# Performance work log

Measured on AMD Instinct MI355X. Metric: run time of the kernel, lower is better.

The kernel has to match this reference:

```python
import jax, jax.numpy as jnp
import numpy as np

B, C, H, W = 4, 64, 128, 128
O, K = 64, 3
STRIDE, PAD = 1, 1
K2 = K * K


def conv2d(x, w, b):
    out = jax.lax.conv_general_dilated(
        x, w, (STRIDE, STRIDE), [(PAD, PAD), (PAD, PAD)],
        dimension_numbers=('NCHW', 'OIHW', 'NCHW'))
    return out + b[None, :, None, None]


def setup_inputs() -> dict:
    key = jax.random.key(0)
    ks = jax.random.split(key, 6)
    return {
        'x': jax.random.normal(ks[0], (B, C, H, W), jnp.float32),
        'offset_w': jax.random.normal(ks[1], (2 * K2, C, K, K), jnp.float32) * 0.01,
        'offset_b': jax.random.normal(ks[2], (2 * K2,), jnp.float32) * 0.01,
        'mask_w': jax.random.normal(ks[3], (K2, C, K, K), jnp.float32) * 0.01,
        'mask_b': jnp.zeros((K2,), jnp.float32),
        'deform_w': jax.random.normal(ks[4], (O, C, K, K), jnp.float32) * (1.0 / np.sqrt(C * K2)),
        'deform_b': jax.random.normal(ks[5], (O,), jnp.float32) * 0.01,
    }


def _deform_conv(x, offset, mask, w, b):
    Bn, Cn, Hin, Win = x.shape
    Ho, Wo = offset.shape[2], offset.shape[3]
    off = offset.reshape(Bn, K2, 2, Ho, Wo)
    ky = jnp.repeat(jnp.arange(K), K)   # kernel row offset per location k
    kx = jnp.tile(jnp.arange(K), K)     # kernel col offset per location k
    yo = jnp.arange(Ho) * STRIDE - PAD
    xo = jnp.arange(Wo) * STRIDE - PAD
    # sampling positions [B,K2,Ho,Wo]
    py = off[:, :, 0] + ky[None, :, None, None] + yo[None, None, :, None]
    px = off[:, :, 1] + kx[None, :, None, None] + xo[None, None, None, :]
    y0 = jnp.floor(py)
    x0 = jnp.floor(px)
    wy1 = py - y0  # fractional weights
    wx1 = px - x0
    y0i = y0.astype(jnp.int32)
    x0i = x0.astype(jnp.int32)
    x_flat = x.reshape(Bn, Cn, Hin * Win)

    def corner(yi, xi, wgt):
        valid = (yi >= 0) & (yi < Hin) & (xi >= 0) & (xi < Win)
        yc = jnp.clip(yi, 0, Hin - 1)
        xc = jnp.clip(xi, 0, Win - 1)
        idx = (yc * Win + xc).reshape(Bn, -1)
        g = jnp.take_along_axis(x_flat, idx[:, None, :], axis=2)
        g = g.reshape(Bn, Cn, K2, Ho, Wo)
        return g * (wgt * valid)[:, None]

    val = (corner(y0i, x0i, (1 - wy1) * (1 - wx1))
           + corner(y0i, x0i + 1, (1 - wy1) * wx1)
           + corner(y0i + 1, x0i, wy1 * (1 - wx1))
           + corner(y0i + 1, x0i + 1, wy1 * wx1))
    val = val * mask[:, None]  # modulate, broadcast over channels
    out = jnp.einsum('bckhw,ock->bohw', val, w.reshape(w.shape[0], Cn, K2))
    return out + b[None, :, None, None]


def reference(x, offset_w, offset_b, mask_w, mask_b, deform_w, deform_b):
    offset = conv2d(x, offset_w, offset_b)
    mask = jax.nn.sigmoid(conv2d(x, mask_w, mask_b))
    return _deform_conv(x, offset, mask, deform_w, deform_b)
```

## Files before the change

kernel.cpp:

```cpp
#include <hip/hip_runtime.h>
#include <hip/hip_bf16.h>
#include <math.h>

#define BB 4
#define CC 64
#define HH 128
#define WW 128
#define HW 16384
#define CHW (CC*HW)

typedef __bf16 bf16;
typedef __attribute__((ext_vector_type(8))) __bf16 bf16x8;
typedef __attribute__((ext_vector_type(4))) __bf16 bf16x4;
typedef __attribute__((ext_vector_type(4))) float f32x4;
typedef __attribute__((ext_vector_type(4))) unsigned short u16x4;

#define MFMA(a, b, c) __builtin_amdgcn_mfma_f32_16x16x32_bf16((a), (b), (c), 0, 0, 0)

__global__ __launch_bounds__(256) void k_pre(const float* __restrict__ x,
        bf16* __restrict__ xt,
        const float* __restrict__ dw, const float* __restrict__ ow,
        const float* __restrict__ mw,
        bf16* __restrict__ wfd_hi, bf16* __restrict__ wfd_lo,
        bf16* __restrict__ wfo_hi, bf16* __restrict__ wfo_lo) {
    __shared__ float tile[64][65];
    if (blockIdx.x < 1024) {
        int b    = blockIdx.x >> 8;
        int s0   = (blockIdx.x & 255) * 64;
        int lane = threadIdx.x & 63;
        int w    = threadIdx.x >> 6;
        const float* xb = x + (size_t)b * CHW;
        #pragma unroll
        for (int r = 0; r < 16; ++r) {
            int c = w * 16 + r;
            tile[c][lane] = xb[(size_t)c * HW + s0 + lane];
        }
        __syncthreads();
        bf16* xtb = xt + (size_t)b * CHW;
        #pragma unroll
        for (int r = 0; r < 16; ++r) {
            int si = w * 16 + r;
            xtb[(size_t)(s0 + si) * 64 + lane] = (bf16)tile[lane][si];
        }
    } else {
        int idx = (blockIdx.x - 1024) * 256 + threadIdx.x;
        if (idx < 36864) {
            int j    = idx & 7;
            int lane = (idx >> 3) & 63;
            int ks   = (idx >> 9) % 18;
            int nt   = idx / (512 * 18);
            int n    = nt * 16 + (lane & 15);
            int kglob = ks * 32 + (lane >> 4) * 8 + j;
            int kk = kglob >> 6, c = kglob & 63;
            float w = dw[(n * 64 + c) * 9 + kk];
            bf16 h = (bf16)w;
            wfd_hi[idx] = h;
            wfd_lo[idx] = (bf16)(w - (float)h);
        } else {
            int idx2 = idx - 36864;
            int j    = idx2 & 7;
            int lane = (idx2 >> 3) & 63;
            int ks   = (idx2 >> 9) % 18;
            int nt   = idx2 / (512 * 18);
            int ch   = nt * 16 + (lane & 15);
            int kglob = ks * 32 + (lane >> 4) * 8 + j;
            int kk = kglob >> 6, c = kglob & 63;
            float w = 0.0f;
            if (ch < 18)      w = ow[(ch * 64 + c) * 9 + kk];
            else if (ch < 27) w = mw[((ch - 18) * 64 + c) * 9 + kk];
            bf16 h = (bf16)w;
            wfo_hi[idx2] = h;
            wfo_lo[idx2] = (bf16)(w - (float)h);
        }
    }
}

__global__ __launch_bounds__(256) void k_fused(const bf16* __restrict__ xt,
        const bf16* __restrict__ wfo_hi, const bf16* __restrict__ wfo_lo,
        const bf16* __restrict__ wfd_hi,
        const float* __restrict__ ob, const float* __restrict__ mb,
        const float* __restrict__ db, float* __restrict__ out) {
    __shared__ __align__(16) bf16 a_s[18 * 64 * 8];
    __shared__ float om_s[27 * 64];
    __shared__ __align__(8) bf16 sampw[576 * 4];
    __shared__ __align__(8) unsigned short sampo[576 * 4];

    int pos0 = blockIdx.x * 64;
    int wo0 = pos0 & 127;
    int ho  = (pos0 >> 7) & 127;
    int b   = pos0 >> 14;
    int t = threadIdx.x, wave = t >> 6, lane = t & 63;
    int m = lane & 15, g = lane >> 4;
    const bf16* xtb = xt + (size_t)b * CHW;

    {
        int st = wave;
        f32x4 acc0 = {0.f, 0.f, 0.f, 0.f};
        f32x4 acc1 = {0.f, 0.f, 0.f, 0.f};
        const bf16x8* bh0 = (const bf16x8*)wfo_hi + lane;
        const bf16x8* bl0 = (const bf16x8*)wfo_lo + lane;
        const bf16x8* bh1 = (const bf16x8*)wfo_hi + 18 * 64 + lane;
        const bf16x8* bl1 = (const bf16x8*)wfo_lo + 18 * 64 + lane;
        #pragma unroll
        for (int kk = 0; kk < 9; ++kk) {
            int y  = ho + kk / 3 - 1;
            int xx = wo0 + st * 16 + m + (kk % 3) - 1;
            bf16x8 ae = {};
            bf16x8 ao = {};
            if ((unsigned)y < 128u && (unsigned)xx < 128u) {
                const bf16* bp = xtb + ((size_t)(y * 128 + xx) << 6);
                ae = *(const bf16x8*)(bp + g * 8);
                ao = *(const bf16x8*)(bp + 32 + g * 8);
            }
            int ks0 = 2 * kk, ks1 = 2 * kk + 1;
            acc0 = MFMA(ae, bh0[ks0 * 64], acc0);
            acc0 = MFMA(ae, bl0[ks0 * 64], acc0);
            acc0 = MFMA(ao, bh0[ks1 * 64], acc0);
            acc0 = MFMA(ao, bl0[ks1 * 64], acc0);
            acc1 = MFMA(ae, bh1[ks0 * 64], acc1);
            acc1 = MFMA(ae, bl1[ks0 * 64], acc1);
            acc1 = MFMA(ao, bh1[ks1 * 64], acc1);
            acc1 = MFMA(ao, bl1[ks1 * 64], acc1);
        }
        int p64 = st * 16 + g * 4;
        float bias0 = ob[m];
        #pragma unroll
        for (int r = 0; r < 4; ++r)
            om_s[m * 64 + p64 + r] = acc0[r] + bias0;
        int ch1 = 16 + m;
        if (ch1 < 27) {
            float bias1 = (ch1 < 18) ? ob[ch1] : mb[ch1 - 18];
            #pragma unroll
            for (int r = 0; r < 4; ++r) {
                float v = acc1[r] + bias1;
                if (ch1 >= 18) v = 1.0f / (1.0f + __expf(-v));
                om_s[ch1 * 64 + p64 + r] = v;
            }
        }
    }
    __syncthreads();

    for (int task = t; task < 576; task += 256) {
        int p64 = task / 9, k = task - p64 * 9;
        float dy = om_s[(2 * k) * 64 + p64];
        float dx = om_s[(2 * k + 1) * 64 + p64];
        float mk = om_s[(18 + k) * 64 + p64];
        float py = (float)(ho - 1 + k / 3) + dy;
        float px = (float)(wo0 + p64 - 1 + (k % 3)) + dx;
        float y0f = floorf(py), x0f = floorf(px);
        float fy = py - y0f, fx = px - x0f;
        int y0 = (int)y0f, x0 = (int)x0f;
        int y1 = y0 + 1,  x1 = x0 + 1;
        bool vy0 = (unsigned)y0 < 128u, vy1 = (unsigned)y1 < 128u;
        bool vx0 = (unsigned)x0 < 128u, vx1 = (unsigned)x1 < 128u;
        int y0c = min(max(y0, 0), 127), y1c = min(max(y1, 0), 127);
        int x0c = min(max(x0, 0), 127), x1c = min(max(x1, 0), 127);
        bf16x4 wv;
        wv.x = (bf16)((vy0 && vx0) ? mk * (1.f - fy) * (1.f - fx) : 0.f);
        wv.y = (bf16)((vy0 && vx1) ? mk * (1.f - fy) * fx         : 0.f);
        wv.z = (bf16)((vy1 && vx0) ? mk * fy * (1.f - fx)         : 0.f);
        wv.w = (bf16)((vy1 && vx1) ? mk * fy * fx                 : 0.f);
        u16x4 ov;
        ov.x = (unsigned short)(y0c * 128 + x0c);
        ov.y = (unsigned short)(y0c * 128 + x1c);
        ov.z = (unsigned short)(y1c * 128 + x0c);
        ov.w = (unsigned short)(y1c * 128 + x1c);
        *(bf16x4*)&sampw[task * 4] = wv;
        *(u16x4*)&sampo[task * 4] = ov;
    }
    __syncthreads();

    const bf16x8* bhd = (const bf16x8*)wfd_hi + (size_t)wave * 18 * 64 + lane;
    int c4 = m * 4;
    int p = wave * 4 + g;
    int gch = (c4 & 31) >> 3;
    int kpar = c4 >> 5;
    int fle = ((m ^ g) + (g << 4)) * 8;
    int flo = ((m ^ g ^ 4) + (g << 4)) * 8;

    for (int st = 0; st < 4; ++st) {
        int taskbase = (st * 16 + p) * 9;
        #pragma unroll
        for (int kk = 0; kk < 9; ++kk) {
            int task = taskbase + kk;
            bf16x4 wb = *(const bf16x4*)&sampw[task * 4];
            u16x4  o4 = *(const u16x4*)&sampo[task * 4];
            bf16x4 v00 = *(const bf16x4*)&xtb[((int)o4.x << 6) + c4];
            bf16x4 v01 = *(const bf16x4*)&xtb[((int)o4.y << 6) + c4];
            bf16x4 v10 = *(const bf16x4*)&xtb[((int)o4.z << 6) + c4];
            bf16x4 v11 = *(const bf16x4*)&xtb[((int)o4.w << 6) + c4];
            float w00 = (float)wb.x, w01 = (float)wb.y;
            float w10 = (float)wb.z, w11 = (float)wb.w;
            float r0 = w00 * (float)v00.x + w01 * (float)v01.x + w10 * (float)v10.x + w11 * (float)v11.x;
            float r1 = w00 * (float)v00.y + w01 * (float)v01.y + w10 * (float)v10.y + w11 * (float)v11.y;
            float r2 = w00 * (float)v00.z + w01 * (float)v01.z + w10 * (float)v10.z + w11 * (float)v11.z;
            float r3 = w00 * (float)v00.w + w01 * (float)v01.w + w10 * (float)v10.w + w11 * (float)v11.w;
            int ks = 2 * kk + kpar;
            int fl = (p ^ gch ^ ((ks & 1) << 2)) + (gch << 4);
            bf16x4 hv = {(bf16)r0, (bf16)r1, (bf16)r2, (bf16)r3};
            *(bf16x4*)((char*)a_s + (((ks * 64 + fl) << 4) + ((c4 & 7) << 1))) = hv;
        }
        __syncthreads();

        f32x4 acc = {0.f, 0.f, 0.f, 0.f};
        #pragma unroll
        for (int kk = 0; kk < 9; ++kk) {
            bf16x8 a0 = *(const bf16x8*)&a_s[(2 * kk) * 512 + fle];
            bf16x8 a1 = *(const bf16x8*)&a_s[(2 * kk + 1) * 512 + flo];
            acc = MFMA(a0, bhd[(2 * kk) * 64], acc);
            acc = MFMA(a1, bhd[(2 * kk + 1) * 64], acc);
        }
        int o = wave * 16 + m;
        float bias = db[o];
        float4 vv = {acc[0] + bias, acc[1] + bias, acc[2] + bias, acc[3] + bias};
        *(float4*)&out[((size_t)(b * 64 + o)) * HW + ho * 128 + wo0 + st * 16 + g * 4] = vv;
        if (st < 3) __syncthreads();
    }
}

extern "C" void kernel_launch(void* const* d_in, const int* in_sizes, int n_in,
                              void* d_out, int out_size, void* d_ws, size_t ws_size,
                              hipStream_t stream) {
    const float* x   = (const float*)d_in[0];
    const float* ow  = (const float*)d_in[1];
    const float* ob  = (const float*)d_in[2];
    const float* mw  = (const float*)d_in[3];
    const float* mb  = (const float*)d_in[4];
    const float* dw  = (const float*)d_in[5];
    const float* db  = (const float*)d_in[6];
    float* out = (float*)d_out;

    bf16* xt = (bf16*)d_ws;
    bf16* wfd_hi = xt + (size_t)BB * HW * CC;
    bf16* wfd_lo = wfd_hi + 36864;
    bf16* wfo_hi = wfd_lo + 36864;
    bf16* wfo_lo = wfo_hi + 18432;

    k_pre<<<1024 + 216, 256, 0, stream>>>(x, xt, dw, ow, mw, wfd_hi, wfd_lo, wfo_hi, wfo_lo);
    k_fused<<<(BB * HW) / 64, 256, 0, stream>>>(xt, wfo_hi, wfo_lo, wfd_hi, ob, mb, db, out);
}
```

Before: 127.5 us.

## Feed sampled values straight into MFMA registers, dropping LDS staging of the A tile

The deform-conv stage now has each wave own one 16-position strip and compute all four output-channel tiles. Each lane gathers 8-channel bf16 vectors and builds the MFMA A fragment directly in registers, which removes the a_s LDS buffer and the per-strip barriers. The transpose pre-kernel also moves to float4 loads and 16-byte bf16 stores, and the unused wfd_lo buffer is no longer produced. Launch bounds now request 4 blocks per CU, which can raise register pressure from the four accumulators and wider gather vectors.

```diff
diff --git a/kernel.cpp b/kernel.cpp
--- a/kernel.cpp
+++ b/kernel.cpp
@@ -21,27 +21,38 @@
         bf16* __restrict__ xt,
         const float* __restrict__ dw, const float* __restrict__ ow,
         const float* __restrict__ mw,
-        bf16* __restrict__ wfd_hi, bf16* __restrict__ wfd_lo,
+        bf16* __restrict__ wfd_hi,
         bf16* __restrict__ wfo_hi, bf16* __restrict__ wfo_lo) {
     __shared__ float tile[64][65];
     if (blockIdx.x < 1024) {
-        int b    = blockIdx.x >> 8;
-        int s0   = (blockIdx.x & 255) * 64;
-        int lane = threadIdx.x & 63;
-        int w    = threadIdx.x >> 6;
+        int b  = blockIdx.x >> 8;
+        int s0 = (blockIdx.x & 255) * 64;
+        int t  = threadIdx.x;
         const float* xb = x + (size_t)b * CHW;
-        #pragma unroll
-        for (int r = 0; r < 16; ++r) {
-            int c = w * 16 + r;
-            tile[c][lane] = xb[(size_t)c * HW + s0 + lane];
+        int sl = (t & 15) * 4;
+        int c0 = t >> 4;
+        #pragma unroll
+        for (int r = 0; r < 4; ++r) {
+            int c = c0 + r * 16;
+            float4 v = *(const float4*)&xb[(size_t)c * HW + s0 + sl];
+            tile[c][sl]     = v.x;
+            tile[c][sl + 1] = v.y;
+            tile[c][sl + 2] = v.z;
+            tile[c][sl + 3] = v.w;
         }
         __syncthreads();
-        bf16* xtb = xt + (size_t)b * CHW;
-        #pragma unroll
-        for (int r = 0; r < 16; ++r) {
-            int si = w * 16 + r;
-            xtb[(size_t)(s0 + si) * 64 + lane] = (bf16)tile[lane][si];
-        }
+        int lane = t & 63, w = t >> 6;
+        int si = w * 16 + (lane >> 2);
+        int cg = (lane & 3) * 16;
+        bf16x8 h0, h1;
+        #pragma unroll
+        for (int j = 0; j < 8; ++j) {
+            h0[j] = (bf16)tile[cg + j][si];
+            h1[j] = (bf16)tile[cg + 8 + j][si];
+        }
+        bf16* dst = xt + (size_t)b * CHW + (size_t)(s0 + si) * 64 + cg;
+        *(bf16x8*)dst       = h0;
+        *(bf16x8*)(dst + 8) = h1;
     } else {
         int idx = (blockIdx.x - 1024) * 256 + threadIdx.x;
         if (idx < 36864) {
@@ -52,10 +63,7 @@
             int n    = nt * 16 + (lane & 15);
             int kglob = ks * 32 + (lane >> 4) * 8 + j;
             int kk = kglob >> 6, c = kglob & 63;
-            float w = dw[(n * 64 + c) * 9 + kk];
-            bf16 h = (bf16)w;
-            wfd_hi[idx] = h;
-            wfd_lo[idx] = (bf16)(w - (float)h);
+            wfd_hi[idx] = (bf16)dw[(n * 64 + c) * 9 + kk];
         } else {
             int idx2 = idx - 36864;
             int j    = idx2 & 7;
@@ -75,12 +83,11 @@
     }
 }
 
-__global__ __launch_bounds__(256) void k_fused(const bf16* __restrict__ xt,
+__global__ __launch_bounds__(256, 4) void k_fused(const bf16* __restrict__ xt,
         const bf16* __restrict__ wfo_hi, const bf16* __restrict__ wfo_lo,
         const bf16* __restrict__ wfd_hi,
         const float* __restrict__ ob, const float* __restrict__ mb,
         const float* __restrict__ db, float* __restrict__ out) {
-    __shared__ __align__(16) bf16 a_s[18 * 64 * 8];
     __shared__ float om_s[27 * 64];
     __shared__ __align__(8) bf16 sampw[576 * 4];
     __shared__ __align__(8) unsigned short sampo[576 * 4];
@@ -170,51 +177,59 @@
     }
     __syncthreads();
 
-    const bf16x8* bhd = (const bf16x8*)wfd_hi + (size_t)wave * 18 * 64 + lane;
-    int c4 = m * 4;
-    int p = wave * 4 + g;
-    int gch = (c4 & 31) >> 3;
-    int kpar = c4 >> 5;
-    int fle = ((m ^ g) + (g << 4)) * 8;
-    int flo = ((m ^ g ^ 4) + (g << 4)) * 8;
-
-    for (int st = 0; st < 4; ++st) {
-        int taskbase = (st * 16 + p) * 9;
+    {
+        int st = wave;
+        f32x4 acc[4];
+        #pragma unroll
+        for (int nt = 0; nt < 4; ++nt) acc[nt] = (f32x4){0.f, 0.f, 0.f, 0.f};
+        const bf16x8* bhd = (const bf16x8*)wfd_hi + lane;
+        int taskbase = (st * 16 + m) * 9;
+        int cb0 = g * 8;
+        int cb1 = 32 + g * 8;
         #pragma unroll
         for (int kk = 0; kk < 9; ++kk) {
             int task = taskbase + kk;
             bf16x4 wb = *(const bf16x4*)&sampw[task * 4];
             u16x4  o4 = *(const u16x4*)&sampo[task * 4];
-            bf16x4 v00 = *(const bf16x4*)&xtb[((int)o4.x << 6) + c4];
-            bf16x4 v01 = *(const bf16x4*)&xtb[((int)o4.y << 6) + c4];
-            bf16x4 v10 = *(const bf16x4*)&xtb[((int)o4.z << 6) + c4];
-            bf16x4 v11 = *(const bf16x4*)&xtb[((int)o4.w << 6) + c4];
             float w00 = (float)wb.x, w01 = (float)wb.y;
             float w10 = (float)wb.z, w11 = (float)wb.w;
-            float r0 = w00 * (float)v00.x + w01 * (float)v01.x + w10 * (float)v10.x + w11 * (float)v11.x;
-            float r1 = w00 * (float)v00.y + w01 * (float)v01.y + w10 * (float)v10.y + w11 * (float)v11.y;
-            float r2 = w00 * (float)v00.z + w01 * (float)v01.z + w10 * (float)v10.z + w11 * (float)v11.z;
-            float r3 = w00 * (float)v00.w + w01 * (float)v01.w + w10 * (float)v10.w + w11 * (float)v11.w;
-            int ks = 2 * kk + kpar;
-            int fl = (p ^ gch ^ ((ks & 1) << 2)) + (gch << 4);
-            bf16x4 hv = {(bf16)r0, (bf16)r1, (bf16)r2, (bf16)r3};
-            *(bf16x4*)((char*)a_s + (((ks * 64 + fl) << 4) + ((c4 & 7) << 1))) = hv;
-        }
-        __syncthreads();
-
-        f32x4 acc = {0.f, 0.f, 0.f, 0.f};
-        #pragma unroll
-        for (int kk = 0; kk < 9; ++kk) {
-            bf16x8 a0 = *(const bf16x8*)&a_s[(2 * kk) * 512 + fle];
-            bf16x8 a1 = *(const bf16x8*)&a_s[(2 * kk + 1) * 512 + flo];
-            acc = MFMA(a0, bhd[(2 * kk) * 64], acc);
-            acc = MFMA(a1, bhd[(2 * kk + 1) * 64], acc);
-        }
-        int o = wave * 16 + m;
-        float bias = db[o];
-        float4 vv = {acc[0] + bias, acc[1] + bias, acc[2] + bias, acc[3] + bias};
-        *(float4*)&out[((size_t)(b * 64 + o)) * HW + ho * 128 + wo0 + st * 16 + g * 4] = vv;
-        if (st < 3) __syncthreads();
+            const bf16* p00 = xtb + ((int)o4.x << 6);
+            const bf16* p01 = xtb + ((int)o4.y << 6);
+            const bf16* p10 = xtb + ((int)o4.z << 6);
+            const bf16* p11 = xtb + ((int)o4.w << 6);
+            bf16x8 e00 = *(const bf16x8*)(p00 + cb0);
+            bf16x8 e01 = *(const bf16x8*)(p01 + cb0);
+            bf16x8 e10 = *(const bf16x8*)(p10 + cb0);
+            bf16x8 e11 = *(const bf16x8*)(p11 + cb0);
+            bf16x8 d00 = *(const bf16x8*)(p00 + cb1);
+            bf16x8 d01 = *(const bf16x8*)(p01 + cb1);
+            bf16x8 d10 = *(const bf16x8*)(p10 + cb1);
+            bf16x8 d11 = *(const bf16x8*)(p11 + cb1);
+            bf16x8 a0, a1;
+            #pragma unroll
+            for (int j = 0; j < 8; ++j) {
+                float r0 = w00 * (float)e00[j] + w01 * (float)e01[j]
+                         + w10 * (float)e10[j] + w11 * (float)e11[j];
+                float r1 = w00 * (float)d00[j] + w01 * (float)d01[j]
+                         + w10 * (float)d10[j] + w11 * (float)d11[j];
+                a0[j] = (bf16)r0;
+                a1[j] = (bf16)r1;
+            }
+            int ks0 = 2 * kk, ks1 = 2 * kk + 1;
+            #pragma unroll
+            for (int nt = 0; nt < 4; ++nt) {
+                acc[nt] = MFMA(a0, bhd[(nt * 18 + ks0) * 64], acc[nt]);
+                acc[nt] = MFMA(a1, bhd[(nt * 18 + ks1) * 64], acc[nt]);
+            }
+        }
+        #pragma unroll
+        for (int nt = 0; nt < 4; ++nt) {
+            int o = nt * 16 + m;
+            float bias = db[o];
+            float4 vv = {acc[nt][0] + bias, acc[nt][1] + bias,
+                         acc[nt][2] + bias, acc[nt][3] + bias};
+            *(float4*)&out[((size_t)(b * 64 + o)) * HW + ho * 128 + wo0 + st * 16 + g * 4] = vv;
+        }
     }
 }
 
@@ -232,10 +247,9 @@
 
     bf16* xt = (bf16*)d_ws;
     bf16* wfd_hi = xt + (size_t)BB * HW * CC;
-    bf16* wfd_lo = wfd_hi + 36864;
-    bf16* wfo_hi = wfd_lo + 36864;
+    bf16* wfo_hi = wfd_hi + 36864;
     bf16* wfo_lo = wfo_hi + 18432;
 
-    k_pre<<<1024 + 216, 256, 0, stream>>>(x, xt, dw, ow, mw, wfd_hi, wfd_lo, wfo_hi, wfo_lo);
+    k_pre<<<1024 + 216, 256, 0, stream>>>(x, xt, dw, ow, mw, wfd_hi, wfo_hi, wfo_lo);
     k_fused<<<(BB * HW) / 64, 256, 0, stream>>>(xt, wfo_hi, wfo_lo, wfd_hi, ob, mb, db, out);
 }
```

Result: slower. 140.2 us (+10.0%).
